# Optimization experiments

Hardware: AMD Instinct MI355X
Metric: run time of the kernel (lower is better)

The kernel has to match this reference:

```python
import jax, jax.numpy as jnp
import numpy as np

N_NODES = 50000
C = 128
E = 800000
B = 4096
NEG = 5
NUM_LAYERS = 3


def setup_inputs() -> dict:
    key = jax.random.key(0)
    ks = jax.random.split(key, 8)
    edge_index = jax.random.randint(ks[0], (2, E), 0, N_NODES, dtype=jnp.int64)
    edge_weight = jax.random.uniform(ks[1], (E,), dtype=jnp.float32)
    n_id = jax.random.randint(ks[2], ((2 + NEG) * B,), 0, N_NODES, dtype=jnp.int64)
    x = jnp.zeros((1,), jnp.float32)  # ignored by forward (overwritten by id_embed)
    id_embed = jax.random.normal(ks[3], (N_NODES, C), jnp.float32) * 0.1
    w1 = jax.random.normal(ks[4], (2 * C, C), jnp.float32) * (1.0 / np.sqrt(2 * C))
    b1 = jnp.zeros((C,), jnp.float32)
    w2 = jax.random.normal(ks[5], (C, 1), jnp.float32) * (1.0 / np.sqrt(C))
    b2 = jnp.zeros((1,), jnp.float32)
    return {"x": x, "edge_index": edge_index, "edge_weight": edge_weight,
            "n_id": n_id, "neg_sample_num": NEG, "id_embed": id_embed,
            "w1": w1, "b1": b1, "w2": w2, "b2": b2}


def reference(x, edge_index, edge_weight, n_id, neg_sample_num, id_embed, w1, b1, w2, b2):
    n_nodes = id_embed.shape[0]
    row, col = edge_index[0], edge_index[1]
    # symmetric GCN normalization (LGCConv)
    deg = jax.ops.segment_sum(jnp.ones_like(row, dtype=id_embed.dtype), row,
                              num_segments=n_nodes)
    dinv = jnp.where(deg > 0, jax.lax.rsqrt(jnp.maximum(deg, 1e-12)), 0.0)
    norm = (dinv[row] * dinv[col])[:, None]  # [E,1]
    h = id_embed
    final = id_embed
    for _ in range(NUM_LAYERS):
        h = jax.ops.segment_sum(norm * h[col], row, num_segments=n_nodes)
        final = final + h
    final = final / (NUM_LAYERS + 1)
    # split n_id into (out, pos, neg) index groups
    b = n_id.shape[0] // (2 + neg_sample_num)
    out = final[n_id[:b]]
    pos = final[n_id[b:2 * b]]
    neg = final[n_id[2 * b:]]
    tiled_out = jnp.repeat(out, neg_sample_num, axis=0)  # [b*neg, C]

    def pred_head(z):  # Linear -> LeakyReLU(0.2) -> (Dropout eval=identity) -> Linear
        z = jax.nn.leaky_relu(z @ w1 + b1, negative_slope=0.2)
        return z @ w2 + b2

    pos_logit = pred_head(jnp.concatenate([out, pos], axis=-1))
    neg_logits = pred_head(jnp.concatenate([tiled_out, neg], axis=-1))
    return pos_logit, neg_logits
```

## Files before the change

### kernel.cpp

```cpp
#include <hip/hip_runtime.h>
#include <hip/hip_bf16.h>

#define C 128
#define NBKT 128
#define BCAP 8192

typedef __bf16 bf16x8 __attribute__((ext_vector_type(8)));
typedef float floatx4 __attribute__((ext_vector_type(4)));

__device__ __forceinline__ unsigned short f2bf(float f) {
    unsigned u = __float_as_uint(f);
    unsigned r = (u + 0x7FFFu + ((u >> 16) & 1u)) >> 16;
    return (unsigned short)r;
}
__device__ __forceinline__ float bflo(unsigned v) { return __uint_as_float(v << 16); }
__device__ __forceinline__ float bfhi(unsigned v) { return __uint_as_float(v & 0xFFFF0000u); }
__device__ __forceinline__ unsigned packbf(float lo, float hi) {
    return (unsigned)f2bf(lo) | ((unsigned)f2bf(hi) << 16);
}

__device__ __forceinline__ int g_idx(const void* p, long long i, int is64) {
    if (is64) return (int)((const long long*)p)[i];
    return ((const int*)p)[i];
}
__device__ __forceinline__ float g_flt(const void* p, long long i, int isf32) {
    if (isf32) return ((const float*)p)[i];
    return __uint_as_float(((unsigned)((const unsigned short*)p)[i]) << 16);
}

__global__ void k_detect(const void* edge, const void* nid, const void* emb, int* flags,
                         unsigned* g0, unsigned* g1, unsigned* g2, int* bucketcnt, int N) {
    int t = threadIdx.x;
    int buf = t >> 6, w = t & 63;
    size_t o = (size_t)N * 64 + w;
    if (buf == 0) g0[o] = 0;
    else if (buf == 1) g1[o] = 0;
    else g2[o] = 0;
    if (t < NBKT) bucketcnt[t] = 0;
    if (t < 64) {
        const unsigned* wrd = (const unsigned*)edge;
        const unsigned* nw = (const unsigned*)nid;
        int predA = (t < 32) ? (wrd[2 * t + 1] == 0u) : 1;
        int predB = (t < 32) ? (nw[2 * t + 1] == 0u) : 1;
        const unsigned short* h = (const unsigned short*)emb;
        int ex = (h[2 * t] >> 7) & 0xFF;
        int plaus = (ex >= 0x6C && ex <= 0x7F) ? 1 : 0;
        unsigned long long mA = __ballot(predA);
        unsigned long long mB = __ballot(predB);
        unsigned long long mP = __ballot(plaus);
        if (t == 0) {
            flags[0] = (mA == ~0ull) ? 1 : 0;
            flags[1] = (mB == ~0ull) ? 1 : 0;
            flags[2] = (__popcll(mP) < 32) ? 1 : 0;
        }
    }
}

__global__ void k_bucketA(const void* edge, int E, int rpb, const int* flags,
                          unsigned* __restrict__ bucketbuf, int* __restrict__ bucketcnt) {
    __shared__ int lcnt[NBKT];
    __shared__ int lbase[NBKT];
    int t = threadIdx.x;
    int is64 = flags[0];
    const int PER = 8;
    int chunkSz = blockDim.x * PER;
    long long stride = (long long)gridDim.x * chunkSz;
    for (long long base = (long long)blockIdx.x * chunkSz; base < E; base += stride) {
        if (t < NBKT) lcnt[t] = 0;
        __syncthreads();
        int bkt[PER], rank[PER];
        unsigned enc[PER];
#pragma unroll
        for (int j = 0; j < PER; ++j) {
            long long e = base + (long long)j * blockDim.x + t;
            if (e < E) {
                int r = g_idx(edge, e, is64);
                int c = g_idx(edge, (long long)E + e, is64);
                int b = r / rpb;
                bkt[j] = b;
                enc[j] = ((unsigned)(r - b * rpb) << 16) | (unsigned)(c & 0xFFFF);
                rank[j] = atomicAdd(&lcnt[b], 1);
            } else bkt[j] = -1;
        }
        __syncthreads();
        if (t < NBKT) lbase[t] = atomicAdd(&bucketcnt[t], lcnt[t]);
        __syncthreads();
#pragma unroll
        for (int j = 0; j < PER; ++j) {
            if (bkt[j] >= 0) {
                int pos = lbase[bkt[j]] + rank[j];
                if (pos < BCAP)
                    bucketbuf[(size_t)bkt[j] * BCAP + pos] = enc[j];
            }
        }
    }
}

__global__ __launch_bounds__(512) void k_bsort(
        const unsigned* __restrict__ bucketbuf, const int* __restrict__ bucketcnt,
        int* __restrict__ rowptr, float* __restrict__ dinv, float* __restrict__ di2,
        float* __restrict__ rdinv, unsigned short* __restrict__ cols16, int N, int rpb) {
    __shared__ int hist[512];
    int b = blockIdx.x;
    int t = threadIdx.x;
    int base = 0, cnt = 0, total = 0;
    for (int i = 0; i < NBKT; ++i) {
        int v = bucketcnt[i];
        if (v > BCAP) v = BCAP;
        if (i < b) base += v;
        if (i == b) cnt = v;
        total += v;
    }
    int r0 = b * rpb;
    int rows = N - r0;
    if (rows > rpb) rows = rpb;
    if (rows < 0) rows = 0;

    hist[t] = 0;
    __syncthreads();
    const unsigned* buf = bucketbuf + (size_t)b * BCAP;
    for (int i = t; i < cnt; i += 512) atomicAdd(&hist[buf[i] >> 16], 1);
    __syncthreads();
    int v = hist[t];
    __syncthreads();
    for (int off = 1; off < 512; off <<= 1) {
        int x = (t >= off) ? hist[t - off] : 0;
        __syncthreads();
        hist[t] += x;
        __syncthreads();
    }
    int excl = hist[t] - v;
    if (t < rows) {
        int r = r0 + t;
        rowptr[r] = base + excl;
        float fd = (float)v;
        float dv = (v > 0) ? rsqrtf(fd) : 0.0f;
        dinv[r] = dv;
        di2[r] = dv * dv;
        rdinv[r] = (v > 0) ? sqrtf(fd) : 0.0f;
    }
    if (b == NBKT - 1 && t == 0) rowptr[N] = total;
    __syncthreads();
    hist[t] = base + excl;
    __syncthreads();
    for (int i = t; i < cnt; i += 512) {
        unsigned u = buf[i];
        int pos = atomicAdd(&hist[u >> 16], 1);
        cols16[pos] = (unsigned short)(u & 0xFFFF);
    }
}

__global__ void k_init(const void* emb, const float* __restrict__ dinv,
                       unsigned* __restrict__ h0, unsigned* __restrict__ g0,
                       int n2, const int* flags) {
    int i = blockIdx.x * blockDim.x + threadIdx.x;
    if (i < n2) {
        int f32 = flags[2];
        float lo = g_flt(emb, 2LL * i, f32);
        float hi = g_flt(emb, 2LL * i + 1, f32);
        h0[i] = packbf(lo, hi);
        float dv = dinv[i >> 6];
        g0[i] = packbf(lo * dv, hi * dv);
    }
}

__global__ void k_layer(const int* __restrict__ rowptr, const unsigned short* __restrict__ cols16,
                        const uint4* __restrict__ gin, uint4* __restrict__ gout,
                        const float* __restrict__ di2, int N) {
    int node = blockIdx.x * (blockDim.x >> 6) + (threadIdx.x >> 6);
    if (node >= N) return;
    int lane = threadIdx.x & 63;
    int quad = lane >> 4, l16 = lane & 15;
    int p = rowptr[node];
    int end = rowptr[node + 1];
    float a0 = 0.f, a1 = 0.f, a2 = 0.f, a3 = 0.f;
    float a4 = 0.f, a5 = 0.f, a6 = 0.f, a7 = 0.f;
    for (int base = p; base < end; base += 8) {
        int ia = base + quad;
        int ib = base + 4 + quad;
        int ca = cols16[ia];
        int cb = cols16[ib];
        ca = (ia < end) ? ca : N;
        cb = (ib < end) ? cb : N;
        uint4 va = gin[(size_t)ca * 16 + l16];
        uint4 vb = gin[(size_t)cb * 16 + l16];
        a0 += bflo(va.x) + bflo(vb.x); a1 += bfhi(va.x) + bfhi(vb.x);
        a2 += bflo(va.y) + bflo(vb.y); a3 += bfhi(va.y) + bfhi(vb.y);
        a4 += bflo(va.z) + bflo(vb.z); a5 += bfhi(va.z) + bfhi(vb.z);
        a6 += bflo(va.w) + bflo(vb.w); a7 += bfhi(va.w) + bfhi(vb.w);
    }
    a0 += __shfl_xor(a0, 16, 64); a0 += __shfl_xor(a0, 32, 64);
    a1 += __shfl_xor(a1, 16, 64); a1 += __shfl_xor(a1, 32, 64);
    a2 += __shfl_xor(a2, 16, 64); a2 += __shfl_xor(a2, 32, 64);
    a3 += __shfl_xor(a3, 16, 64); a3 += __shfl_xor(a3, 32, 64);
    a4 += __shfl_xor(a4, 16, 64); a4 += __shfl_xor(a4, 32, 64);
    a5 += __shfl_xor(a5, 16, 64); a5 += __shfl_xor(a5, 32, 64);
    a6 += __shfl_xor(a6, 16, 64); a6 += __shfl_xor(a6, 32, 64);
    a7 += __shfl_xor(a7, 16, 64); a7 += __shfl_xor(a7, 32, 64);
    if (quad == 0) {
        float s = di2[node];
        uint4 o;
        o.x = packbf(a0 * s, a1 * s);
        o.y = packbf(a2 * s, a3 * s);
        o.z = packbf(a4 * s, a5 * s);
        o.w = packbf(a6 * s, a7 * s);
        gout[(size_t)node * 16 + l16] = o;
    }
}

__global__ void k_layer3(const int* __restrict__ rowptr, const unsigned short* __restrict__ cols16,
                         const uint4* __restrict__ gin , const uint4* __restrict__ h0,
                         const uint4* __restrict__ g1, uint4* __restrict__ fin,
                         const float* __restrict__ di2, const float* __restrict__ rdinv, int N) {
    int node = blockIdx.x * (blockDim.x >> 6) + (threadIdx.x >> 6);
    if (node >= N) return;
    int lane = threadIdx.x & 63;
    int quad = lane >> 4, l16 = lane & 15;
    int p = rowptr[node];
    int end = rowptr[node + 1];
    float a0 = 0.f, a1 = 0.f, a2 = 0.f, a3 = 0.f;
    float a4 = 0.f, a5 = 0.f, a6 = 0.f, a7 = 0.f;
    for (int base = p; base < end; base += 8) {
        int ia = base + quad;
        int ib = base + 4 + quad;
        int ca = cols16[ia];
        int cb = cols16[ib];
        ca = (ia < end) ? ca : N;
        cb = (ib < end) ? cb : N;
        uint4 va = gin[(size_t)ca * 16 + l16];
        uint4 vb = gin[(size_t)cb * 16 + l16];
        a0 += bflo(va.x) + bflo(vb.x); a1 += bfhi(va.x) + bfhi(vb.x);
        a2 += bflo(va.y) + bflo(vb.y); a3 += bfhi(va.y) + bfhi(vb.y);
        a4 += bflo(va.z) + bflo(vb.z); a5 += bfhi(va.z) + bfhi(vb.z);
        a6 += bflo(va.w) + bflo(vb.w); a7 += bfhi(va.w) + bfhi(vb.w);
    }
    a0 += __shfl_xor(a0, 16, 64); a0 += __shfl_xor(a0, 32, 64);
    a1 += __shfl_xor(a1, 16, 64); a1 += __shfl_xor(a1, 32, 64);
    a2 += __shfl_xor(a2, 16, 64); a2 += __shfl_xor(a2, 32, 64);
    a3 += __shfl_xor(a3, 16, 64); a3 += __shfl_xor(a3, 32, 64);
    a4 += __shfl_xor(a4, 16, 64); a4 += __shfl_xor(a4, 32, 64);
    a5 += __shfl_xor(a5, 16, 64); a5 += __shfl_xor(a5, 32, 64);
    a6 += __shfl_xor(a6, 16, 64); a6 += __shfl_xor(a6, 32, 64);
    a7 += __shfl_xor(a7, 16, 64); a7 += __shfl_xor(a7, 32, 64);
    if (quad == 0) {
        float s = di2[node];
        float rd = rdinv[node];
        size_t ro = (size_t)node * 16 + l16;
        uint4 x0 = h0[ro];
        uint4 x1 = g1[ro];
        uint4 x2 = gin[ro];
        uint4 o;
        o.x = packbf(0.25f * (bflo(x0.x) + rd * (bflo(x1.x) + bflo(x2.x) + s * a0)),
                     0.25f * (bfhi(x0.x) + rd * (bfhi(x1.x) + bfhi(x2.x) + s * a1)));
        o.y = packbf(0.25f * (bflo(x0.y) + rd * (bflo(x1.y) + bflo(x2.y) + s * a2)),
                     0.25f * (bfhi(x0.y) + rd * (bfhi(x1.y) + bfhi(x2.y) + s * a3)));
        o.z = packbf(0.25f * (bflo(x0.z) + rd * (bflo(x1.z) + bflo(x2.z) + s * a4)),
                     0.25f * (bfhi(x0.z) + rd * (bfhi(x1.z) + bfhi(x2.z) + s * a5)));
        o.w = packbf(0.25f * (bflo(x0.w) + rd * (bflo(x1.w) + bflo(x2.w) + s * a6)),
                     0.25f * (bfhi(x0.w) + rd * (bfhi(x1.w) + bfhi(x2.w) + s * a7)));
        fin[ro] = o;
    }
}

__global__ void k_prep(const void* w1, const void* b1, const void* w2, const void* b2,
                       unsigned short* __restrict__ w1t, float* __restrict__ b1f,
                       float* __restrict__ w2f, float* __restrict__ b2f, const int* flags) {
    int i = blockIdx.x * blockDim.x + threadIdx.x;
    int f32 = flags[2];
    if (i < 256 * 128) {
        int k = i >> 7, n = i & 127;
        float v = g_flt(w1, i, f32);
        w1t[n * 256 + k] = f2bf(v);
    }
    if (i < 128) {
        b1f[i] = g_flt(b1, i, f32);
        w2f[i] = g_flt(w2, i, f32);
    }
    if (i == 0) b2f[0] = g_flt(b2, 0, f32);
}

__global__ void k_head(const unsigned* __restrict__ fin, const void* n_id,
                       const unsigned short* __restrict__ w1t,
                       const float* __restrict__ b1f, const float* __restrict__ w2f,
                       const float* __restrict__ b2f,
                       float* __restrict__ out, int B, int NEG, const int* flags) {
    __shared__ unsigned short z[64][264];
    int t = threadIdx.x;
    int id64 = flags[1];
    int mbase = blockIdx.x * 64;

    int tu = t & 63;
    int sel = t >> 6;
    int moff = sel >> 1, half = sel & 1;
    for (int m = 0; m < 64; m += 2) {
        int gm = mbase + m + moff;
        int r;
        if (gm < B) {
            r = half ? g_idx(n_id, B + gm, id64) : g_idx(n_id, gm, id64);
        } else {
            int j = gm - B;
            r = half ? g_idx(n_id, 2 * B + j, id64) : g_idx(n_id, j / NEG, id64);
        }
        ((unsigned*)&z[m + moff][0])[half * 64 + tu] = fin[(size_t)r * 64 + tu];
    }
    __syncthreads();

    int wave = t >> 6, lane = t & 63;
    int quad = lane >> 4, l16 = lane & 15;

    floatx4 acc[8] = {};
    bf16x8 a[8];
    const unsigned short* zrow = &z[wave * 16 + l16][0];
#pragma unroll
    for (int ks = 0; ks < 8; ++ks)
        a[ks] = *(const bf16x8*)(zrow + ks * 32 + quad * 8);

#pragma unroll
    for (int ks = 0; ks < 8; ++ks) {
#pragma unroll
        for (int nt = 0; nt < 8; ++nt) {
            bf16x8 b = *(const bf16x8*)(w1t + (nt * 16 + l16) * 256 + ks * 32 + quad * 8);
            acc[nt] = __builtin_amdgcn_mfma_f32_16x16x32_bf16(a[ks], b, acc[nt], 0, 0, 0);
        }
    }

    float s0 = 0.f, s1 = 0.f, s2 = 0.f, s3 = 0.f;
#pragma unroll
    for (int nt = 0; nt < 8; ++nt) {
        int col = nt * 16 + l16;
        float bb = b1f[col], ww = w2f[col];
        float v0 = acc[nt][0] + bb; v0 = (v0 > 0.f) ? v0 : 0.2f * v0; s0 += v0 * ww;
        float v1 = acc[nt][1] + bb; v1 = (v1 > 0.f) ? v1 : 0.2f * v1; s1 += v1 * ww;
        float v2 = acc[nt][2] + bb; v2 = (v2 > 0.f) ? v2 : 0.2f * v2; s2 += v2 * ww;
        float v3 = acc[nt][3] + bb; v3 = (v3 > 0.f) ? v3 : 0.2f * v3; s3 += v3 * ww;
    }
#pragma unroll
    for (int off = 1; off <= 8; off <<= 1) {
        s0 += __shfl_xor(s0, off, 64);
        s1 += __shfl_xor(s1, off, 64);
        s2 += __shfl_xor(s2, off, 64);
        s3 += __shfl_xor(s3, off, 64);
    }
    if (l16 == 0) {
        int rowbase = mbase + wave * 16 + quad * 4;
        float bb2 = b2f[0];
        out[rowbase + 0] = s0 + bb2;
        out[rowbase + 1] = s1 + bb2;
        out[rowbase + 2] = s2 + bb2;
        out[rowbase + 3] = s3 + bb2;
    }
}

extern "C" void kernel_launch(void* const* d_in, const int* in_sizes, int n_in,
                              void* d_out, int out_size, void* d_ws, size_t ws_size,
                              hipStream_t stream) {
    const void* edge_index = d_in[1];
    const void* n_id       = d_in[3];
    const void* id_embed   = d_in[5];
    const void* w1 = d_in[6];
    const void* b1 = d_in[7];
    const void* w2 = d_in[8];
    const void* b2 = d_in[9];
    float* out = (float*)d_out;

    const int E  = in_sizes[1] / 2;
    const int N  = in_sizes[5] / C;
    const int NEG = 5;
    const int B  = in_sizes[3] / (2 + NEG);
    const int n_out_rows = B + B * NEG;
    const int NB = (N + 1) * 64;
    const int rpb = (N + NBKT - 1) / NBKT;

    size_t off = 0;
    auto alloc = [&](size_t nf) {
        char* p = (char*)d_ws + off * 4;
        off += (nf + 255) & ~(size_t)255;
        return p;
    };
    int*   flags     = (int*)alloc(8);
    int*   bucketcnt = (int*)alloc(NBKT);
    float* dinv      = (float*)alloc(N);
    float* di2       = (float*)alloc(N);
    float* rdinv     = (float*)alloc(N);
    int*   rowptr    = (int*)alloc(N + 1);
    unsigned short* cols16 = (unsigned short*)alloc(((size_t)E + 8 + 1) / 2);
    unsigned* bucketbuf = (unsigned*)alloc((size_t)NBKT * BCAP);
    unsigned* h0     = (unsigned*)alloc(NB);
    unsigned* g0     = (unsigned*)alloc(NB);
    unsigned* g1     = (unsigned*)alloc(NB);
    unsigned* g2     = (unsigned*)alloc(NB);
    unsigned* fin    = (unsigned*)alloc((size_t)N * 64);
    unsigned short* w1t = (unsigned short*)alloc(256 * 128 / 2);
    float* b1f       = (float*)alloc(C);
    float* w2f       = (float*)alloc(C);
    float* b2f       = (float*)alloc(8);

    const int BS = 256;
    k_detect<<<1, 192, 0, stream>>>(edge_index, n_id, id_embed, flags, g0, g1, g2, bucketcnt, N);
    const int gridA = (E + BS * 8 - 1) / (BS * 8);
    k_bucketA<<<gridA, BS, 0, stream>>>(edge_index, E, rpb, flags, bucketbuf, bucketcnt);
    k_bsort<<<NBKT, 512, 0, stream>>>(bucketbuf, bucketcnt, rowptr, dinv, di2, rdinv,
                                      cols16, N, rpb);
    k_init<<<(N * 64 + BS - 1) / BS, BS, 0, stream>>>(id_embed, dinv, h0, g0, N * 64, flags);
    k_prep<<<(256 * 128 + BS - 1) / BS, BS, 0, stream>>>(w1, b1, w2, b2, w1t, b1f, w2f, b2f, flags);

    const int waves_per_block = BS / 64;
    const int layer_grid = (N + waves_per_block - 1) / waves_per_block;
    k_layer<<<layer_grid, BS, 0, stream>>>(rowptr, cols16, (const uint4*)g0, (uint4*)g1, di2, N);
    k_layer<<<layer_grid, BS, 0, stream>>>(rowptr, cols16, (const uint4*)g1, (uint4*)g2, di2, N);
    k_layer3<<<layer_grid, BS, 0, stream>>>(rowptr, cols16, (const uint4*)g2, (const uint4*)h0,
                                            (const uint4*)g1, (uint4*)fin, di2, rdinv, N);

    k_head<<<n_out_rows / 64, BS, 0, stream>>>(fin, n_id, w1t, b1f, w2f, b2f, out, B, NEG, flags);
}
```

Measured before the change: 258.2 us.

## Split feature buffers into four column slices so SpMM gathers stay cache-resident

Node feature buffers are reorganized into four 32-column slices, each stored contiguously. Each layer block now handles one slice for four nodes, with 16 edges per wave iteration and 4 lanes per 64-byte row piece, so the gathered working set per slice is a quarter of the table and fits better in L2/MALL. The separate weight-prep kernel is also folded into the init kernel to drop a launch. In exchange, each wave reads 64-byte fragments instead of 256-byte rows, there are four times as many blocks, each one re-reads rowptr and cols for its node, and the reduction needs more shuffle steps.

```diff
diff --git a/kernel.cpp b/kernel.cpp
--- a/kernel.cpp
+++ b/kernel.cpp
@@ -4,6 +4,7 @@
 #define C 128
 #define NBKT 128
 #define BCAP 8192
+#define NSLC 4
 
 typedef __bf16 bf16x8 __attribute__((ext_vector_type(8)));
 typedef float floatx4 __attribute__((ext_vector_type(4)));
@@ -29,10 +30,12 @@
 }
 
 __global__ void k_detect(const void* edge, const void* nid, const void* emb, int* flags,
-                         unsigned* g0, unsigned* g1, unsigned* g2, int* bucketcnt, int N) {
+                         unsigned* g0, unsigned* g1, unsigned* g2, int* bucketcnt,
+                         int N, int SST) {
     int t = threadIdx.x;
     int buf = t >> 6, w = t & 63;
-    size_t o = (size_t)N * 64 + w;
+    int slice = w >> 4, j = w & 15;
+    size_t o = (size_t)slice * SST + (size_t)N * 16 + j;
     if (buf == 0) g0[o] = 0;
     else if (buf == 1) g1[o] = 0;
     else g2[o] = 0;
@@ -150,102 +153,122 @@
     }
 }
 
-__global__ void k_init(const void* emb, const float* __restrict__ dinv,
-                       unsigned* __restrict__ h0, unsigned* __restrict__ g0,
-                       int n2, const int* flags) {
+__global__ void k_initprep(const void* emb, const float* __restrict__ dinv,
+                           unsigned* __restrict__ h0, unsigned* __restrict__ g0,
+                           int n2, int SST,
+                           const void* w1, const void* b1, const void* w2, const void* b2,
+                           unsigned short* __restrict__ w1t, float* __restrict__ b1f,
+                           float* __restrict__ w2f, float* __restrict__ b2f, const int* flags) {
     int i = blockIdx.x * blockDim.x + threadIdx.x;
+    int f32 = flags[2];
     if (i < n2) {
-        int f32 = flags[2];
         float lo = g_flt(emb, 2LL * i, f32);
         float hi = g_flt(emb, 2LL * i + 1, f32);
-        h0[i] = packbf(lo, hi);
-        float dv = dinv[i >> 6];
-        g0[i] = packbf(lo * dv, hi * dv);
-    }
+        int n = i >> 6, w = i & 63;
+        size_t o = (size_t)(w >> 4) * SST + (size_t)n * 16 + (w & 15);
+        h0[o] = packbf(lo, hi);
+        float dv = dinv[n];
+        g0[o] = packbf(lo * dv, hi * dv);
+    }
+    if (i < 256 * 128) {
+        int k = i >> 7, n = i & 127;
+        w1t[n * 256 + k] = f2bf(g_flt(w1, i, f32));
+    }
+    if (i < 128) {
+        b1f[i] = g_flt(b1, i, f32);
+        w2f[i] = g_flt(w2, i, f32);
+    }
+    if (i == 0) b2f[0] = g_flt(b2, 0, f32);
 }
 
 __global__ void k_layer(const int* __restrict__ rowptr, const unsigned short* __restrict__ cols16,
                         const uint4* __restrict__ gin, uint4* __restrict__ gout,
-                        const float* __restrict__ di2, int N) {
-    int node = blockIdx.x * (blockDim.x >> 6) + (threadIdx.x >> 6);
+                        const float* __restrict__ di2, int N, int SST4) {
+    int wave = threadIdx.x >> 6;
+    int slice = blockIdx.x & 3;
+    int node = (blockIdx.x >> 2) * 4 + wave;
     if (node >= N) return;
     int lane = threadIdx.x & 63;
-    int quad = lane >> 4, l16 = lane & 15;
+    int g = lane >> 2, q = lane & 3;
+    const uint4* gs = gin + (size_t)slice * SST4;
     int p = rowptr[node];
     int end = rowptr[node + 1];
     float a0 = 0.f, a1 = 0.f, a2 = 0.f, a3 = 0.f;
     float a4 = 0.f, a5 = 0.f, a6 = 0.f, a7 = 0.f;
-    for (int base = p; base < end; base += 8) {
-        int ia = base + quad;
-        int ib = base + 4 + quad;
-        int ca = cols16[ia];
-        int cb = cols16[ib];
-        ca = (ia < end) ? ca : N;
-        cb = (ib < end) ? cb : N;
-        uint4 va = gin[(size_t)ca * 16 + l16];
-        uint4 vb = gin[(size_t)cb * 16 + l16];
-        a0 += bflo(va.x) + bflo(vb.x); a1 += bfhi(va.x) + bfhi(vb.x);
-        a2 += bflo(va.y) + bflo(vb.y); a3 += bfhi(va.y) + bfhi(vb.y);
-        a4 += bflo(va.z) + bflo(vb.z); a5 += bfhi(va.z) + bfhi(vb.z);
-        a6 += bflo(va.w) + bflo(vb.w); a7 += bfhi(va.w) + bfhi(vb.w);
-    }
-    a0 += __shfl_xor(a0, 16, 64); a0 += __shfl_xor(a0, 32, 64);
-    a1 += __shfl_xor(a1, 16, 64); a1 += __shfl_xor(a1, 32, 64);
-    a2 += __shfl_xor(a2, 16, 64); a2 += __shfl_xor(a2, 32, 64);
-    a3 += __shfl_xor(a3, 16, 64); a3 += __shfl_xor(a3, 32, 64);
-    a4 += __shfl_xor(a4, 16, 64); a4 += __shfl_xor(a4, 32, 64);
-    a5 += __shfl_xor(a5, 16, 64); a5 += __shfl_xor(a5, 32, 64);
-    a6 += __shfl_xor(a6, 16, 64); a6 += __shfl_xor(a6, 32, 64);
-    a7 += __shfl_xor(a7, 16, 64); a7 += __shfl_xor(a7, 32, 64);
-    if (quad == 0) {
+    for (int base = p; base < end; base += 16) {
+        int idx = base + g;
+        int c = cols16[idx];
+        c = (idx < end) ? c : N;
+        uint4 v = gs[(size_t)c * 4 + q];
+        a0 += bflo(v.x); a1 += bfhi(v.x);
+        a2 += bflo(v.y); a3 += bfhi(v.y);
+        a4 += bflo(v.z); a5 += bfhi(v.z);
+        a6 += bflo(v.w); a7 += bfhi(v.w);
+    }
+#pragma unroll
+    for (int off = 4; off <= 32; off <<= 1) {
+        a0 += __shfl_xor(a0, off, 64);
+        a1 += __shfl_xor(a1, off, 64);
+        a2 += __shfl_xor(a2, off, 64);
+        a3 += __shfl_xor(a3, off, 64);
+        a4 += __shfl_xor(a4, off, 64);
+        a5 += __shfl_xor(a5, off, 64);
+        a6 += __shfl_xor(a6, off, 64);
+        a7 += __shfl_xor(a7, off, 64);
+    }
+    if (g == 0) {
         float s = di2[node];
         uint4 o;
         o.x = packbf(a0 * s, a1 * s);
         o.y = packbf(a2 * s, a3 * s);
         o.z = packbf(a4 * s, a5 * s);
         o.w = packbf(a6 * s, a7 * s);
-        gout[(size_t)node * 16 + l16] = o;
+        gout[(size_t)slice * SST4 + (size_t)node * 4 + q] = o;
     }
 }
 
 __global__ void k_layer3(const int* __restrict__ rowptr, const unsigned short* __restrict__ cols16,
                          const uint4* __restrict__ gin , const uint4* __restrict__ h0,
                          const uint4* __restrict__ g1, uint4* __restrict__ fin,
-                         const float* __restrict__ di2, const float* __restrict__ rdinv, int N) {
-    int node = blockIdx.x * (blockDim.x >> 6) + (threadIdx.x >> 6);
+                         const float* __restrict__ di2, const float* __restrict__ rdinv,
+                         int N, int SST4) {
+    int wave = threadIdx.x >> 6;
+    int slice = blockIdx.x & 3;
+    int node = (blockIdx.x >> 2) * 4 + wave;
     if (node >= N) return;
     int lane = threadIdx.x & 63;
-    int quad = lane >> 4, l16 = lane & 15;
+    int g = lane >> 2, q = lane & 3;
+    size_t sb = (size_t)slice * SST4;
+    const uint4* gs = gin + sb;
     int p = rowptr[node];
     int end = rowptr[node + 1];
     float a0 = 0.f, a1 = 0.f, a2 = 0.f, a3 = 0.f;
     float a4 = 0.f, a5 = 0.f, a6 = 0.f, a7 = 0.f;
-    for (int base = p; base < end; base += 8) {
-        int ia = base + quad;
-        int ib = base + 4 + quad;
-        int ca = cols16[ia];
-        int cb = cols16[ib];
-        ca = (ia < end) ? ca : N;
-        cb = (ib < end) ? cb : N;
-        uint4 va = gin[(size_t)ca * 16 + l16];
-        uint4 vb = gin[(size_t)cb * 16 + l16];
-        a0 += bflo(va.x) + bflo(vb.x); a1 += bfhi(va.x) + bfhi(vb.x);
-        a2 += bflo(va.y) + bflo(vb.y); a3 += bfhi(va.y) + bfhi(vb.y);
-        a4 += bflo(va.z) + bflo(vb.z); a5 += bfhi(va.z) + bfhi(vb.z);
-        a6 += bflo(va.w) + bflo(vb.w); a7 += bfhi(va.w) + bfhi(vb.w);
-    }
-    a0 += __shfl_xor(a0, 16, 64); a0 += __shfl_xor(a0, 32, 64);
-    a1 += __shfl_xor(a1, 16, 64); a1 += __shfl_xor(a1, 32, 64);
-    a2 += __shfl_xor(a2, 16, 64); a2 += __shfl_xor(a2, 32, 64);
-    a3 += __shfl_xor(a3, 16, 64); a3 += __shfl_xor(a3, 32, 64);
-    a4 += __shfl_xor(a4, 16, 64); a4 += __shfl_xor(a4, 32, 64);
-    a5 += __shfl_xor(a5, 16, 64); a5 += __shfl_xor(a5, 32, 64);
-    a6 += __shfl_xor(a6, 16, 64); a6 += __shfl_xor(a6, 32, 64);
-    a7 += __shfl_xor(a7, 16, 64); a7 += __shfl_xor(a7, 32, 64);
-    if (quad == 0) {
+    for (int base = p; base < end; base += 16) {
+        int idx = base + g;
+        int c = cols16[idx];
+        c = (idx < end) ? c : N;
+        uint4 v = gs[(size_t)c * 4 + q];
+        a0 += bflo(v.x); a1 += bfhi(v.x);
+        a2 += bflo(v.y); a3 += bfhi(v.y);
+        a4 += bflo(v.z); a5 += bfhi(v.z);
+        a6 += bflo(v.w); a7 += bfhi(v.w);
+    }
+#pragma unroll
+    for (int off = 4; off <= 32; off <<= 1) {
+        a0 += __shfl_xor(a0, off, 64);
+        a1 += __shfl_xor(a1, off, 64);
+        a2 += __shfl_xor(a2, off, 64);
+        a3 += __shfl_xor(a3, off, 64);
+        a4 += __shfl_xor(a4, off, 64);
+        a5 += __shfl_xor(a5, off, 64);
+        a6 += __shfl_xor(a6, off, 64);
+        a7 += __shfl_xor(a7, off, 64);
+    }
+    if (g == 0) {
         float s = di2[node];
         float rd = rdinv[node];
-        size_t ro = (size_t)node * 16 + l16;
+        size_t ro = sb + (size_t)node * 4 + q;
         uint4 x0 = h0[ro];
         uint4 x1 = g1[ro];
         uint4 x2 = gin[ro];
@@ -258,25 +281,8 @@
                      0.25f * (bfhi(x0.z) + rd * (bfhi(x1.z) + bfhi(x2.z) + s * a5)));
         o.w = packbf(0.25f * (bflo(x0.w) + rd * (bflo(x1.w) + bflo(x2.w) + s * a6)),
                      0.25f * (bfhi(x0.w) + rd * (bfhi(x1.w) + bfhi(x2.w) + s * a7)));
-        fin[ro] = o;
-    }
-}
-
-__global__ void k_prep(const void* w1, const void* b1, const void* w2, const void* b2,
-                       unsigned short* __restrict__ w1t, float* __restrict__ b1f,
-                       float* __restrict__ w2f, float* __restrict__ b2f, const int* flags) {
-    int i = blockIdx.x * blockDim.x + threadIdx.x;
-    int f32 = flags[2];
-    if (i < 256 * 128) {
-        int k = i >> 7, n = i & 127;
-        float v = g_flt(w1, i, f32);
-        w1t[n * 256 + k] = f2bf(v);
-    }
-    if (i < 128) {
-        b1f[i] = g_flt(b1, i, f32);
-        w2f[i] = g_flt(w2, i, f32);
-    }
-    if (i == 0) b2f[0] = g_flt(b2, 0, f32);
+        fin[(size_t)node * 16 + slice * 4 + q] = o;
+    }
 }
 
 __global__ void k_head(const unsigned* __restrict__ fin, const void* n_id,
@@ -368,7 +374,9 @@
     const int NEG = 5;
     const int B  = in_sizes[3] / (2 + NEG);
     const int n_out_rows = B + B * NEG;
-    const int NB = (N + 1) * 64;
+    const int SST = (N + 1) * 16;
+    const int SST4 = (N + 1) * 4;
+    const int NB = NSLC * SST;
     const int rpb = (N + NBKT - 1) / NBKT;
 
     size_t off = 0;
@@ -383,7 +391,7 @@
     float* di2       = (float*)alloc(N);
     float* rdinv     = (float*)alloc(N);
     int*   rowptr    = (int*)alloc(N + 1);
-    unsigned short* cols16 = (unsigned short*)alloc(((size_t)E + 8 + 1) / 2);
+    unsigned short* cols16 = (unsigned short*)alloc(((size_t)E + 16 + 1) / 2);
     unsigned* bucketbuf = (unsigned*)alloc((size_t)NBKT * BCAP);
     unsigned* h0     = (unsigned*)alloc(NB);
     unsigned* g0     = (unsigned*)alloc(NB);
@@ -396,20 +404,22 @@
     float* b2f       = (float*)alloc(8);
 
     const int BS = 256;
-    k_detect<<<1, 192, 0, stream>>>(edge_index, n_id, id_embed, flags, g0, g1, g2, bucketcnt, N);
+    k_detect<<<1, 192, 0, stream>>>(edge_index, n_id, id_embed, flags, g0, g1, g2,
+                                    bucketcnt, N, SST);
     const int gridA = (E + BS * 8 - 1) / (BS * 8);
     k_bucketA<<<gridA, BS, 0, stream>>>(edge_index, E, rpb, flags, bucketbuf, bucketcnt);
     k_bsort<<<NBKT, 512, 0, stream>>>(bucketbuf, bucketcnt, rowptr, dinv, di2, rdinv,
                                       cols16, N, rpb);
-    k_init<<<(N * 64 + BS - 1) / BS, BS, 0, stream>>>(id_embed, dinv, h0, g0, N * 64, flags);
-    k_prep<<<(256 * 128 + BS - 1) / BS, BS, 0, stream>>>(w1, b1, w2, b2, w1t, b1f, w2f, b2f, flags);
-
-    const int waves_per_block = BS / 64;
-    const int layer_grid = (N + waves_per_block - 1) / waves_per_block;
-    k_layer<<<layer_grid, BS, 0, stream>>>(rowptr, cols16, (const uint4*)g0, (uint4*)g1, di2, N);
-    k_layer<<<layer_grid, BS, 0, stream>>>(rowptr, cols16, (const uint4*)g1, (uint4*)g2, di2, N);
+    k_initprep<<<(N * 64 + BS - 1) / BS, BS, 0, stream>>>(
+        id_embed, dinv, h0, g0, N * 64, SST, w1, b1, w2, b2, w1t, b1f, w2f, b2f, flags);
+
+    const int layer_grid = ((N + 3) / 4) * NSLC;
+    k_layer<<<layer_grid, BS, 0, stream>>>(rowptr, cols16, (const uint4*)g0, (uint4*)g1,
+                                           di2, N, SST4);
+    k_layer<<<layer_grid, BS, 0, stream>>>(rowptr, cols16, (const uint4*)g1, (uint4*)g2,
+                                           di2, N, SST4);
     k_layer3<<<layer_grid, BS, 0, stream>>>(rowptr, cols16, (const uint4*)g2, (const uint4*)h0,
-                                            (const uint4*)g1, (uint4*)fin, di2, rdinv, N);
+                                            (const uint4*)g1, (uint4*)fin, di2, rdinv, N, SST4);
 
     k_head<<<n_out_rows / 64, BS, 0, stream>>>(fin, n_id, w1t, b1f, w2f, b2f, out, B, NEG, flags);
 }
```

After: 381.2 us. +47.7%, slower.
